# Performance work log

Measured on AMD Instinct MI355X. Metric: run time of the kernel, lower is better.

## Reference

```python
import jax, jax.numpy as jnp
import numpy as np

NUM_HEADS = 16
NUM_KV_HEADS = 4
HEAD_DIM = 256
ROPE_THETA = 10000.0


def _rope(x, position_ids):
    # x: [B, H, S, D], position_ids: [B, S]
    d = x.shape[-1]
    inv_freq = 1.0 / (ROPE_THETA ** (jnp.arange(0, d, 2, dtype=jnp.float32) / d))  # [D/2]
    freqs = position_ids.astype(jnp.float32)[:, :, None] * inv_freq[None, None, :]  # [B, S, D/2]
    emb = jnp.concatenate([freqs, freqs], axis=-1)  # [B, S, D]
    cos = jnp.cos(emb)[:, None, :, :]
    sin = jnp.sin(emb)[:, None, :, :]
    x1, x2 = jnp.split(x, 2, axis=-1)
    rot = jnp.concatenate([-x2, x1], axis=-1)
    return x * cos + rot * sin


def setup_inputs() -> dict:
    key = jax.random.key(0)
    k1, k2, k3, k4, k5 = jax.random.split(key, 5)
    B, S, H = 2, 2048, 2048
    hidden_states = jax.random.normal(k1, (B, S, H), dtype=jnp.float32)
    position_ids = jnp.broadcast_to(jnp.arange(S, dtype=jnp.int32)[None, :], (B, S))
    scale = 1.0 / np.sqrt(H)
    wq = jax.random.normal(k2, (H, NUM_HEADS * HEAD_DIM), dtype=jnp.float32) * scale
    wk = jax.random.normal(k3, (H, NUM_KV_HEADS * HEAD_DIM), dtype=jnp.float32) * scale
    wv = jax.random.normal(k4, (H, NUM_KV_HEADS * HEAD_DIM), dtype=jnp.float32) * scale
    wo = jax.random.normal(k5, (NUM_HEADS * HEAD_DIM, H), dtype=jnp.float32) * (1.0 / np.sqrt(NUM_HEADS * HEAD_DIM))
    return {"hidden_states": hidden_states, "position_ids": position_ids,
            "wq": wq, "wk": wk, "wv": wv, "wo": wo}


def reference(hidden_states, position_ids, wq, wk, wv, wo):
    B, S, H = hidden_states.shape
    groups = NUM_HEADS // NUM_KV_HEADS
    # QKV projections -> [B, heads, S, D]
    q = (hidden_states @ wq).reshape(B, S, NUM_HEADS, HEAD_DIM).transpose(0, 2, 1, 3)
    k = (hidden_states @ wk).reshape(B, S, NUM_KV_HEADS, HEAD_DIM).transpose(0, 2, 1, 3)
    v = (hidden_states @ wv).reshape(B, S, NUM_KV_HEADS, HEAD_DIM).transpose(0, 2, 1, 3)
    q = _rope(q, position_ids)
    k = _rope(k, position_ids)
    # GQA without materializing repeated K/V: group query heads per kv head
    qg = q.reshape(B, NUM_KV_HEADS, groups, S, HEAD_DIM)
    scale = 1.0 / jnp.sqrt(jnp.asarray(HEAD_DIM, dtype=q.dtype))
    scores = jnp.einsum('bkgqd,bkvd->bkgqv', qg, k) * scale  # [B, KV, G, S, S]
    causal = jnp.tril(jnp.ones((S, S), dtype=bool))
    scores = jnp.where(causal[None, None, None, :, :], scores, jnp.finfo(scores.dtype).min)
    probs = jax.nn.softmax(scores, axis=-1)
    out = jnp.einsum('bkgqv,bkvd->bkgqd', probs, v)  # [B, KV, G, S, D]
    out = out.reshape(B, NUM_HEADS, S, HEAD_DIM).transpose(0, 2, 1, 3).reshape(B, S, NUM_HEADS * HEAD_DIM)
    return out @ wo
```

## Files before the change

kernel.cpp:

```cpp
#include <hip/hip_runtime.h>

typedef unsigned short u16;
typedef __bf16 bf16_t;
typedef bf16_t bf16x8 __attribute__((ext_vector_type(8)));
typedef float f32x4 __attribute__((ext_vector_type(4)));
typedef float f32x16 __attribute__((ext_vector_type(16)));

#define LOG2E 1.4426950408889634f
#define QKVS 6144

__device__ __forceinline__ u16 f2bf(float f) {
  union { float f; unsigned u; } c; c.f = f;
  unsigned r = c.u + 0x7fffu + ((c.u >> 16) & 1u);
  return (u16)(r >> 16);
}
__device__ __forceinline__ float bf2f(u16 u) {
  union { unsigned u; float f; } c; c.u = ((unsigned)u) << 16;
  return c.f;
}

__device__ __forceinline__ void gload16(const void* g, void* l) {
  __builtin_amdgcn_global_load_lds(
      (const __attribute__((address_space(1))) unsigned int*)g,
      (__attribute__((address_space(3))) unsigned int*)l, 16, 0, 0);
}

__device__ __forceinline__ unsigned cvtpk(float lo, float hi) {
  unsigned r;
  asm("v_cvt_pk_bf16_f32 %0, %1, %2" : "=v"(r) : "v"(lo), "v"(hi));
  return r;
}
__device__ __forceinline__ void swap32(unsigned& a, unsigned& b) {
  asm("v_permlane32_swap_b32 %0, %1" : "+v"(a), "+v"(b));
}

#define MFMA16(a, b, c) __builtin_amdgcn_mfma_f32_16x16x32_bf16((a), (b), (c), 0, 0, 0)
#define MFMA32(a, b, c) __builtin_amdgcn_mfma_f32_32x32x16_bf16((a), (b), (c), 0, 0, 0)


__global__ __launch_bounds__(256) void k_convert_f32_bf16(const float* __restrict__ in,
                                                          u16* __restrict__ out, int n4) {
  int i = blockIdx.x * 256 + threadIdx.x;
  if (i >= n4) return;
  float4 v = ((const float4*)in)[i];
  ushort4 o;
  o.x = f2bf(v.x); o.y = f2bf(v.y); o.z = f2bf(v.z); o.w = f2bf(v.w);
  ((ushort4*)out)[i] = o;
}

__global__ __launch_bounds__(256) void k_transpose_f32_bf16(const float* __restrict__ in,
                                                            u16* __restrict__ out, int R, int C) {
  __shared__ float tile[32][33];
  int tx = threadIdx.x, ty = threadIdx.y;
  int bx = blockIdx.x * 32, by = blockIdx.y * 32;
#pragma unroll
  for (int i = 0; i < 4; i++)
    tile[ty + i * 8][tx] = in[(size_t)(by + ty + i * 8) * C + bx + tx];
  __syncthreads();
#pragma unroll
  for (int i = 0; i < 4; i++)
    out[(size_t)(bx + ty + i * 8) * R + by + tx] = f2bf(tile[tx][ty + i * 8]);
}

__global__ __launch_bounds__(256) void k_transpose_bf16(const u16* __restrict__ in,
                                                        u16* __restrict__ out, int R, int C) {
  __shared__ u16 tile[32][33];
  int tx = threadIdx.x, ty = threadIdx.y;
  int bx = blockIdx.x * 32, by = blockIdx.y * 32;
#pragma unroll
  for (int i = 0; i < 4; i++)
    tile[ty + i * 8][tx] = in[(size_t)(by + ty + i * 8) * C + bx + tx];
  __syncthreads();
#pragma unroll
  for (int i = 0; i < 4; i++)
    out[(size_t)(bx + ty + i * 8) * R + by + tx] = tile[tx][ty + i * 8];
}

__global__ __launch_bounds__(256) void k_rope(u16* __restrict__ x, const int* __restrict__ pos,
                                              int nh_mask, int nh_shift, int width) {
  int idx = blockIdx.x * 256 + threadIdx.x;
  int i = idx & 127;
  int h = (idx >> 7) & nh_mask;
  int row = idx >> (7 + nh_shift);
  int p = pos[row];
  float f = (float)p * exp2f((float)i * (-13.287712379549449f / 128.f));
  float sn, cs;
  sincosf(f, &sn, &cs);
  size_t base = (size_t)row * width + h * 256 + i;
  float x1 = bf2f(x[base]), x2 = bf2f(x[base + 128]);
  x[base] = f2bf(x1 * cs - x2 * sn);
  x[base + 128] = f2bf(x2 * cs + x1 * sn);
}


template <int OUT_BF16>
__global__ __launch_bounds__(256) void k_gemm_bt(const u16* __restrict__ A,
                                                 const u16* __restrict__ Bt,
                                                 void* __restrict__ C, int M, int N, int K) {
  __shared__ u16 As[128 * 64];
  __shared__ u16 Bs[128 * 64];
  const int tid = threadIdx.x;
  const int lane = tid & 63;
  const int w = tid >> 6;
  const int l15 = lane & 15, l4 = lane >> 4;
  const int wr = w >> 1, wc = w & 1;
  const int bx = blockIdx.x, by = blockIdx.y;

  f32x4 acc[4][4];
#pragma unroll
  for (int a = 0; a < 4; a++)
#pragma unroll
    for (int b2 = 0; b2 < 4; b2++) acc[a][b2] = (f32x4){0.f, 0.f, 0.f, 0.f};

  const u16* Abase = A + (size_t)by * 128 * K;
  const u16* Bbase = Bt + (size_t)bx * 128 * K;

  for (int kk = 0; kk < K; kk += 64) {
    __syncthreads();
#pragma unroll
    for (int j = 0; j < 4; j++) {
      int ci = w * 256 + j * 64 + lane;
      int row = ci >> 3, c = ci & 7;
      gload16(Abase + (size_t)row * K + kk + c * 8, (char*)As + ci * 16);
      gload16(Bbase + (size_t)row * K + kk + c * 8, (char*)Bs + ci * 16);
    }
    __syncthreads();
#pragma unroll
    for (int kc = 0; kc < 2; kc++) {
      int kb = kc * 64 + l4 * 16;
      bf16x8 av[4], bv[4];
#pragma unroll
      for (int mt = 0; mt < 4; mt++)
        av[mt] = *(const bf16x8*)((const char*)As + (wr * 64 + mt * 16 + l15) * 128 + kb);
#pragma unroll
      for (int nt = 0; nt < 4; nt++)
        bv[nt] = *(const bf16x8*)((const char*)Bs + (wc * 64 + nt * 16 + l15) * 128 + kb);
#pragma unroll
      for (int mt = 0; mt < 4; mt++)
#pragma unroll
        for (int nt = 0; nt < 4; nt++) acc[mt][nt] = MFMA16(av[mt], bv[nt], acc[mt][nt]);
    }
  }
#pragma unroll
  for (int mt = 0; mt < 4; mt++) {
#pragma unroll
    for (int nt = 0; nt < 4; nt++) {
      int col = bx * 128 + wc * 64 + nt * 16 + l15;
#pragma unroll
      for (int r = 0; r < 4; r++) {
        int row = by * 128 + wr * 64 + mt * 16 + l4 * 4 + r;
        if (OUT_BF16)
          ((u16*)C)[(size_t)row * N + col] = f2bf(acc[mt][nt][r]);
        else
          ((float*)C)[(size_t)row * N + col] = acc[mt][nt][r];
      }
    }
  }
}


__global__ __launch_bounds__(512, 1) void k_gemm256(const u16* __restrict__ A,
                                                    const u16* __restrict__ Bt,
                                                    u16* __restrict__ C, int N, int K) {
  extern __shared__ char smem[];
  const int tid = threadIdx.x;
  const int lane = tid & 63, w = tid >> 6;
  const int l15 = lane & 15, l4 = lane >> 4;
  const int wr = w >> 2, wc = w & 3;
  const int bx = blockIdx.x, by = blockIdx.y;
  const int NT = K >> 6;

  const u16* Ab = A + (size_t)(by * 256) * K;
  const u16* Bb = Bt + (size_t)(bx * 256) * K;

  int srcoff[2], dstoff[2];
#pragma unroll
  for (int rr = 0; rr < 2; rr++) {
    int ci = rr * 512 + tid;
    int lc = ci ^ (((ci >> 5) & 1) << 1);
    int kc = lc >> 9, row = (lc >> 2) & 127, g2 = lc & 3;
    srcoff[rr] = row * K + kc * 32 + g2 * 8;
    dstoff[rr] = ci * 16;
  }

  auto SH = [&](int Tg, int halfidx) {
    const u16* base = (halfidx < 2) ? (Ab + (size_t)(halfidx * 128) * K)
                                    : (Bb + (size_t)((halfidx - 2) * 128) * K);
    char* dst = smem + (Tg & 1) * 65536 + halfidx * 16384;
    int kk = Tg * 64;
#pragma unroll
    for (int rr = 0; rr < 2; rr++)
      gload16(base + srcoff[rr] + kk, dst + dstoff[rr]);
  };

  auto lda = [&](int c, int kc, int mrow4) -> bf16x8 {
    int L = kc * 8192 + (mrow4 * 16 + l15) * 64 + l4 * 16;
    int P = L ^ (((L >> 9) & 1) << 5);
    return *(const bf16x8*)(smem + c * 65536 + wr * 16384 + P);
  };
  auto ldb = [&](int c, int kc, int j) -> bf16x8 {
    int L = kc * 8192 + ((wc & 1) * 64 + j * 16 + l15) * 64 + l4 * 16;
    int P = L ^ (((L >> 9) & 1) << 5);
    return *(const bf16x8*)(smem + c * 65536 + 32768 + (wc >> 1) * 16384 + P);
  };

  f32x4 acc[8][4];
#pragma unroll
  for (int i = 0; i < 8; i++)
#pragma unroll
    for (int j = 0; j < 4; j++) acc[i][j] = (f32x4){0.f, 0.f, 0.f, 0.f};

  SH(0, 0); SH(0, 1); SH(0, 2); SH(0, 3);
  SH(1, 2); SH(1, 3);
  asm volatile("s_waitcnt vmcnt(4)" ::: "memory");
  __builtin_amdgcn_s_barrier();
  asm volatile("" ::: "memory");

  bf16x8 bv[2][4];
  for (int T = 0; T < NT; ++T) {
    const int c = T & 1;
#pragma unroll
    for (int q = 0; q < 4; q++) {
      const int kc = q & 1, mh = q >> 1;
      bf16x8 av[4];
      if (q < 2) {
#pragma unroll
        for (int j = 0; j < 4; j++) bv[kc][j] = ldb(c, kc, j);
      }
#pragma unroll
      for (int ii = 0; ii < 4; ii++) av[ii] = lda(c, kc, mh * 4 + ii);
      if (q == 0)      { if (T + 1 < NT) SH(T + 1, 0); }
      else if (q == 1) { if (T + 1 < NT) SH(T + 1, 1); }
      else if (q == 2) { if (T + 2 < NT) SH(T + 2, 2); }
      else             { if (T + 2 < NT) SH(T + 2, 3); }
      if (q == 3) {
        if (T < NT - 2)       asm volatile("s_waitcnt vmcnt(4)" ::: "memory");
        else if (T == NT - 2) asm volatile("s_waitcnt vmcnt(0)" ::: "memory");
      }
      asm volatile("" ::: "memory");
      __builtin_amdgcn_s_barrier();
      asm volatile("" ::: "memory");
      asm volatile("s_waitcnt lgkmcnt(0)" ::: "memory");
      __builtin_amdgcn_sched_barrier(0);
      __builtin_amdgcn_s_setprio(1);
#pragma unroll
      for (int ii = 0; ii < 4; ii++)
#pragma unroll
        for (int j = 0; j < 4; j++)
          acc[mh * 4 + ii][j] = MFMA16(av[ii], bv[kc][j], acc[mh * 4 + ii][j]);
      __builtin_amdgcn_s_setprio(0);
      asm volatile("" ::: "memory");
      __builtin_amdgcn_s_barrier();
      asm volatile("" ::: "memory");
    }
  }

#pragma unroll
  for (int i = 0; i < 8; i++) {
#pragma unroll
    for (int j = 0; j < 4; j++) {
      int col = bx * 256 + wc * 64 + j * 16 + l15;
#pragma unroll
      for (int r = 0; r < 4; r++) {
        int row = by * 256 + wr * 128 + i * 16 + l4 * 4 + r;
        C[(size_t)row * N + col] = f2bf(acc[i][j][r]);
      }
    }
  }
}


__shared__ __align__(16) u16 aK0[8192];
__shared__ __align__(16) u16 aK1[8192];
__shared__ __align__(16) u16 aV0[8192];
__shared__ __align__(16) u16 aV1[8192];

__global__ __launch_bounds__(256, 2) void k_attn(const u16* __restrict__ QKV,
                                                 const u16* __restrict__ Vt,
                                                 u16* __restrict__ AO) {
  const int tid = threadIdx.x, lane = tid & 63, w = tid >> 6;
  const int r31 = lane & 31, hi = lane >> 5;

  const int flat = blockIdx.x;
  const int r = flat & 7;
  const int idx = flat >> 3;
  const int b = r >> 2, kv = r & 3;
  const int half = idx >> 5, j = idx & 31;
  const int qb = half ? 15 - (j >> 1) : (j >> 1);
  const int h = kv * 4 + (j & 1) + 2 * half;

  bf16x8 qreg[16];
  {
    const u16* qp = QKV + (size_t)(b * 2048 + qb * 128 + w * 32 + r31) * QKVS + h * 256 + hi * 8;
#pragma unroll
    for (int kc = 0; kc < 16; kc++) qreg[kc] = *(const bf16x8*)(qp + kc * 16);
  }

  f32x16 o[8];
#pragma unroll
  for (int df = 0; df < 8; df++)
#pragma unroll
    for (int jj = 0; jj < 16; jj++) o[df][jj] = 0.f;
  float mrow = -3e38f, lrow = 0.f;

  const int nt = 4 * qb + 4;
  const int tlim = 4 * qb + w;
  const int qloc = qb * 128 + w * 32 + r31;
  const u16* Kbase = QKV + (size_t)(b * 2048) * QKVS + 4096 + kv * 256;
  const u16* Vbase = Vt + (size_t)(kv * 256) * 4096 + b * 2048;

  int kfix[4], vfix[4];
#pragma unroll
  for (int jj = 0; jj < 4; jj++) {
    int ci = jj * 256 + tid;
    int krow = ci >> 5, kc = ci & 31;
    int kcg = (kc & 24) | ((kc ^ krow) & 7);
    kfix[jj] = krow * QKVS + kcg * 8;
    int vrow = ci >> 2, vc = ci & 3;
    int vg = (vc - (vrow >> 1)) & 3;
    vfix[jj] = vrow * 4096 + vg * 8;
  }
  int koff = 0, voff = 0;

  auto STAGE = [&](u16* Kd, u16* Vd) {
#pragma unroll
    for (int jj = 0; jj < 4; jj++)
      gload16(Kbase + kfix[jj] + koff, (char*)Kd + (jj * 256 + tid) * 16);
#pragma unroll
    for (int jj = 0; jj < 4; jj++)
      gload16(Vbase + vfix[jj] + voff, (char*)Vd + (jj * 256 + tid) * 16);
    koff += 32 * QKVS;
    voff += 32;
  };

  auto COMPUTE = [&](int t, const u16* Kc, const u16* Vc) {
    f32x16 s;
#pragma unroll
    for (int jj = 0; jj < 16; jj++) s[jj] = 0.f;
#pragma unroll
    for (int kc = 0; kc < 16; kc++) {
      int ch = kc * 2 + hi;
      int cs = (ch & 24) | ((ch ^ r31) & 7);
      bf16x8 kf = *(const bf16x8*)((const char*)Kc + r31 * 512 + cs * 16);
      s = MFMA32(kf, qreg[kc], s);
    }

    const float C = 0.0625f * LOG2E;
    float z[16];
#pragma unroll
    for (int jj = 0; jj < 16; jj++) z[jj] = s[jj] * C;
    if (t == tlim) {
#pragma unroll
      for (int jj = 0; jj < 16; jj++) {
        int kvg = t * 32 + (jj & 3) + 8 * (jj >> 2) + 4 * hi;
        if (kvg > qloc) z[jj] = -1e30f;
      }
    }

    float m0 = z[0];
#pragma unroll
    for (int jj = 1; jj < 16; jj++) m0 = fmaxf(m0, z[jj]);
    m0 = fmaxf(m0, __shfl_xor(m0, 32));
    if (__any(m0 > mrow + 11.54f)) {
      float mn = fmaxf(mrow, m0);
      float alpha = exp2f(mrow - mn);
      mrow = mn;
      lrow *= alpha;
#pragma unroll
      for (int jj = 0; jj < 16; jj++) {
        float a = __shfl(alpha, (jj & 3) + 8 * (jj >> 2) + 4 * hi);
#pragma unroll
        for (int df = 0; df < 8; df++) o[df][jj] *= a;
      }
    }
    float sum = 0.f;
#pragma unroll
    for (int jj = 0; jj < 16; jj++) {
      z[jj] = exp2f(z[jj] - mrow);
      sum += z[jj];
    }
    sum += __shfl_xor(sum, 32);
    lrow += sum;

    unsigned a0 = cvtpk(z[0], z[1]), a2 = cvtpk(z[4], z[5]);
    swap32(a0, a2);
    unsigned a1 = cvtpk(z[2], z[3]), a3 = cvtpk(z[6], z[7]);
    swap32(a1, a3);
    unsigned b0 = cvtpk(z[8], z[9]), b2 = cvtpk(z[12], z[13]);
    swap32(b0, b2);
    unsigned b1 = cvtpk(z[10], z[11]), b3 = cvtpk(z[14], z[15]);
    swap32(b1, b3);
    union UU { unsigned u[4]; bf16x8 v; };
    UU ua; ua.u[0] = a0; ua.u[1] = a1; ua.u[2] = a2; ua.u[3] = a3;
    UU ub; ub.u[0] = b0; ub.u[1] = b1; ub.u[2] = b2; ub.u[3] = b3;
    bf16x8 pa0 = ua.v, pa1 = ub.v;

#pragma unroll
    for (int df = 0; df < 8; df++) {
      int vr = df * 32 + r31;
      int c0 = (hi + (vr >> 1)) & 3;
      int c1 = (2 + hi + (vr >> 1)) & 3;
      bf16x8 v0 = *(const bf16x8*)((const char*)Vc + vr * 64 + c0 * 16);
      bf16x8 v1 = *(const bf16x8*)((const char*)Vc + vr * 64 + c1 * 16);
      o[df] = MFMA32(pa0, v0, o[df]);
      o[df] = MFMA32(pa1, v1, o[df]);
    }
  };

  STAGE(aK0, aV0);
  __syncthreads();

  for (int t = 0; t < nt; t += 2) {
    STAGE(aK1, aV1);
    if (t <= tlim) COMPUTE(t, aK0, aV0);
    __syncthreads();
    if (t + 2 < nt) STAGE(aK0, aV0);
    if (t + 1 <= tlim) COMPUTE(t + 1, aK1, aV1);
    __syncthreads();
  }

  float rl = 1.f / lrow;
  size_t rowbase = (size_t)(b * 2048 + qb * 128 + w * 32);
#pragma unroll
  for (int jj = 0; jj < 16; jj++) {
    float rr2 = __shfl(rl, (jj & 3) + 8 * (jj >> 2) + 4 * hi);
    int qr = (jj & 3) + 8 * (jj >> 2) + 4 * hi;
#pragma unroll
    for (int df = 0; df < 8; df++)
      AO[(rowbase + qr) * 4096 + h * 256 + df * 32 + r31] = f2bf(o[df][jj] * rr2);
  }
}


#define OFF_AO    0u
#define OFF_XB    0u
#define OFF_WQKVT 16777216u
#define OFF_VT    33554432u
#define OFF_WOT   41943040u
#define OFF_QKV   58720256u

extern "C" void kernel_launch(void* const* d_in, const int* in_sizes, int n_in,
                              void* d_out, int out_size, void* d_ws, size_t ws_size,
                              hipStream_t stream) {
  const float* hs = (const float*)d_in[0];
  const int* pos = (const int*)d_in[1];
  const float* wq = (const float*)d_in[2];
  const float* wk = (const float*)d_in[3];
  const float* wv = (const float*)d_in[4];
  const float* wo = (const float*)d_in[5];
  float* out = (float*)d_out;
  char* ws = (char*)d_ws;

  u16* Xb    = (u16*)(ws + OFF_XB);
  u16* Wqkvt = (u16*)(ws + OFF_WQKVT);
  u16* Vt    = (u16*)(ws + OFF_VT);
  u16* Wot   = (u16*)(ws + OFF_WOT);
  u16* QKV   = (u16*)(ws + OFF_QKV);
  u16* AO    = (u16*)(ws + OFF_AO);

  dim3 tb(32, 8);

  k_convert_f32_bf16<<<8192, 256, 0, stream>>>(hs, Xb, 2097152);
  k_transpose_f32_bf16<<<dim3(128, 64), tb, 0, stream>>>(wq, Wqkvt, 2048, 4096);
  k_transpose_f32_bf16<<<dim3(32, 64), tb, 0, stream>>>(wk, Wqkvt + 4096 * 2048, 2048, 1024);
  k_transpose_f32_bf16<<<dim3(32, 64), tb, 0, stream>>>(wv, Wqkvt + 5120 * 2048, 2048, 1024);
  k_transpose_f32_bf16<<<dim3(64, 128), tb, 0, stream>>>(wo, Wot, 4096, 2048);

  (void)hipFuncSetAttribute((const void*)k_gemm256,
                            hipFuncAttributeMaxDynamicSharedMemorySize, 131072);
  k_gemm256<<<dim3(24, 16), 512, 131072, stream>>>(Xb, Wqkvt, QKV, 6144, 2048);

  k_rope<<<32768, 256, 0, stream>>>(QKV, pos, 15, 4, QKVS);
  k_rope<<<8192, 256, 0, stream>>>(QKV + 4096, pos, 3, 2, QKVS);

  k_transpose_bf16<<<dim3(32, 128), tb, 0, stream>>>(QKV + 5120, Vt, 4096, QKVS);

  k_attn<<<dim3(512), 256, 0, stream>>>(QKV, Vt, AO);

  k_gemm_bt<0><<<dim3(16, 32), 256, 0, stream>>>(AO, Wot, out, 4096, 2048, 4096);
}
```

Baseline: 479.4 us.

## Split heavy causal attention blocks across two wave groups with split-KV merge

The attention kernel now launches 384 blocks of 512 threads instead of 512 blocks of 256. The 256 heavy blocks (query blocks 8-15) split their KV range between two 4-wave groups, each with its own LDS double buffer, and merge the partial softmax states through shared memory at the end. Light blocks (query blocks 0-7) run two heads per block that share one staged KV stream. The aim is to even out the causal load imbalance and the tail effect, at the cost of 128KB of LDS per block, an extra merge step, and occupancy limited to one block per CU.

```diff
diff --git a/kernel.cpp b/kernel.cpp
--- a/kernel.cpp
+++ b/kernel.cpp
@@ -270,24 +270,40 @@
 }
 
 
-__shared__ __align__(16) u16 aK0[8192];
-__shared__ __align__(16) u16 aK1[8192];
-__shared__ __align__(16) u16 aV0[8192];
-__shared__ __align__(16) u16 aV1[8192];
-
-__global__ __launch_bounds__(256, 2) void k_attn(const u16* __restrict__ QKV,
+__global__ __launch_bounds__(512, 1) void k_attn(const u16* __restrict__ QKV,
                                                  const u16* __restrict__ Vt,
                                                  u16* __restrict__ AO) {
-  const int tid = threadIdx.x, lane = tid & 63, w = tid >> 6;
+  __shared__ __align__(16) char sbuf[131072];
+  __shared__ float mlx[256];
+
+  const int tid = threadIdx.x, lane = tid & 63;
+  const int wg = tid >> 6, g = wg >> 2, w = wg & 3;
   const int r31 = lane & 31, hi = lane >> 5;
 
   const int flat = blockIdx.x;
-  const int r = flat & 7;
-  const int idx = flat >> 3;
-  const int b = r >> 2, kv = r & 3;
-  const int half = idx >> 5, j = idx & 31;
-  const int qb = half ? 15 - (j >> 1) : (j >> 1);
-  const int h = kv * 4 + (j & 1) + 2 * half;
+  const bool heavy = flat < 256;
+  int b, kv, qb, h;
+  if (heavy) {
+    int r = flat & 7; b = r >> 2; kv = r & 3;
+    int e = flat >> 3;
+    qb = 15 - (e & 7);
+    h = kv * 4 + (e >> 3);
+  } else {
+    int f2 = flat - 256;
+    int r = f2 & 7; b = r >> 2; kv = r & 3;
+    int e = f2 >> 3;
+    qb = 7 - (e & 7);
+    h = kv * 4 + (e >> 3) * 2 + g;
+  }
+  const int half = heavy ? (2 * qb + 2) : (4 * qb + 4);
+  const int t0 = heavy ? g * half : 0;
+  const bool dostage = heavy || (g == 0);
+
+  char* gb = sbuf + (heavy ? g : 0) * 65536;
+  u16* K0 = (u16*)(gb);
+  u16* K1 = (u16*)(gb + 16384);
+  u16* V0 = (u16*)(gb + 32768);
+  u16* V1 = (u16*)(gb + 49152);
 
   bf16x8 qreg[16];
   {
@@ -303,7 +319,6 @@
     for (int jj = 0; jj < 16; jj++) o[df][jj] = 0.f;
   float mrow = -3e38f, lrow = 0.f;
 
-  const int nt = 4 * qb + 4;
   const int tlim = 4 * qb + w;
   const int qloc = qb * 128 + w * 32 + r31;
   const u16* Kbase = QKV + (size_t)(b * 2048) * QKVS + 4096 + kv * 256;
@@ -312,7 +327,7 @@
   int kfix[4], vfix[4];
 #pragma unroll
   for (int jj = 0; jj < 4; jj++) {
-    int ci = jj * 256 + tid;
+    int ci = jj * 256 + (tid & 255);
     int krow = ci >> 5, kc = ci & 31;
     int kcg = (kc & 24) | ((kc ^ krow) & 7);
     kfix[jj] = krow * QKVS + kcg * 8;
@@ -320,15 +335,15 @@
     int vg = (vc - (vrow >> 1)) & 3;
     vfix[jj] = vrow * 4096 + vg * 8;
   }
-  int koff = 0, voff = 0;
+  int koff = t0 * 32 * QKVS, voff = t0 * 32;
 
   auto STAGE = [&](u16* Kd, u16* Vd) {
 #pragma unroll
     for (int jj = 0; jj < 4; jj++)
-      gload16(Kbase + kfix[jj] + koff, (char*)Kd + (jj * 256 + tid) * 16);
+      gload16(Kbase + kfix[jj] + koff, (char*)Kd + (jj * 256 + (tid & 255)) * 16);
 #pragma unroll
     for (int jj = 0; jj < 4; jj++)
-      gload16(Vbase + vfix[jj] + voff, (char*)Vd + (jj * 256 + tid) * 16);
+      gload16(Vbase + vfix[jj] + voff, (char*)Vd + (jj * 256 + (tid & 255)) * 16);
     koff += 32 * QKVS;
     voff += 32;
   };
@@ -407,27 +422,62 @@
     }
   };
 
-  STAGE(aK0, aV0);
+  if (dostage) STAGE(K0, V0);
   __syncthreads();
 
-  for (int t = 0; t < nt; t += 2) {
-    STAGE(aK1, aV1);
-    if (t <= tlim) COMPUTE(t, aK0, aV0);
+  for (int tt = 0; tt < half; tt += 2) {
+    int t = t0 + tt;
+    if (dostage) STAGE(K1, V1);
+    if (t <= tlim) COMPUTE(t, K0, V0);
     __syncthreads();
-    if (t + 2 < nt) STAGE(aK0, aV0);
-    if (t + 1 <= tlim) COMPUTE(t + 1, aK1, aV1);
+    if (dostage && tt + 2 < half) STAGE(K0, V0);
+    if (t + 1 <= tlim) COMPUTE(t + 1, K1, V1);
     __syncthreads();
   }
 
-  float rl = 1.f / lrow;
-  size_t rowbase = (size_t)(b * 2048 + qb * 128 + w * 32);
-#pragma unroll
-  for (int jj = 0; jj < 16; jj++) {
-    float rr2 = __shfl(rl, (jj & 3) + 8 * (jj >> 2) + 4 * hi);
-    int qr = (jj & 3) + 8 * (jj >> 2) + 4 * hi;
-#pragma unroll
-    for (int df = 0; df < 8; df++)
-      AO[(rowbase + qr) * 4096 + h * 256 + df * 32 + r31] = f2bf(o[df][jj] * rr2);
+  if (!heavy) {
+    float rl = 1.f / lrow;
+    size_t rowbase = (size_t)(b * 2048 + qb * 128 + w * 32);
+#pragma unroll
+    for (int jj = 0; jj < 16; jj++) {
+      float rr2 = __shfl(rl, (jj & 3) + 8 * (jj >> 2) + 4 * hi);
+      int qr = (jj & 3) + 8 * (jj >> 2) + 4 * hi;
+#pragma unroll
+      for (int df = 0; df < 8; df++)
+        AO[(rowbase + qr) * 4096 + h * 256 + df * 32 + r31] = f2bf(o[df][jj] * rr2);
+    }
+  } else {
+    float* X = (float*)sbuf;
+    if (g == 1) {
+      float* xw = X + w * 8192;
+#pragma unroll
+      for (int df = 0; df < 8; df++)
+#pragma unroll
+        for (int jj = 0; jj < 16; jj++) xw[(df * 16 + jj) * 64 + lane] = o[df][jj];
+      if (lane < 32) {
+        mlx[w * 32 + r31] = mrow;
+        mlx[128 + w * 32 + r31] = lrow;
+      }
+    }
+    __syncthreads();
+    if (g == 0) {
+      float m1 = mlx[w * 32 + r31], l1 = mlx[128 + w * 32 + r31];
+      float mm = fmaxf(mrow, m1);
+      float a0 = exp2f(mrow - mm), a1 = exp2f(m1 - mm);
+      float rl = 1.f / (lrow * a0 + l1 * a1);
+      const float* xw = X + w * 8192;
+      size_t rowbase = (size_t)(b * 2048 + qb * 128 + w * 32);
+#pragma unroll
+      for (int jj = 0; jj < 16; jj++) {
+        int qr = (jj & 3) + 8 * (jj >> 2) + 4 * hi;
+        float A0 = __shfl(a0, qr), A1 = __shfl(a1, qr), RL = __shfl(rl, qr);
+#pragma unroll
+        for (int df = 0; df < 8; df++) {
+          float v = o[df][jj] * A0 + xw[(df * 16 + jj) * 64 + lane] * A1;
+          AO[(rowbase + qr) * 4096 + h * 256 + df * 32 + r31] = f2bf(v * RL);
+        }
+      }
+    }
   }
 }
 
@@ -475,7 +525,7 @@
 
   k_transpose_bf16<<<dim3(32, 128), tb, 0, stream>>>(QKV + 5120, Vt, 4096, QKVS);
 
-  k_attn<<<dim3(512), 256, 0, stream>>>(QKV, Vt, AO);
+  k_attn<<<dim3(384), 512, 0, stream>>>(QKV, Vt, AO);
 
   k_gemm_bt<0><<<dim3(16, 32), 256, 0, stream>>>(AO, Wot, out, 4096, 2048, 4096);
 }
```

After: 502.4 us. +4.8%, slower.

## Fuse Q RoPE into attention kernel and batch LDS loads before MFMAs

Applied to the files above, without the earlier changes.

Removes the separate RoPE launch over Q and applies the rotation to the Q registers inside the attention kernel after they are loaded. Each element's frequency and sincos are computed on the fly from the position ids. The QK^T and PV inner loops are also restructured so that eight LDS fragments are loaded before their MFMAs are issued, which should give more latency hiding. The costs are extra transcendental work per attention block and higher register pressure under the launch bound of two blocks per SIMD.

```diff
diff --git a/kernel.cpp b/kernel.cpp
--- a/kernel.cpp
+++ b/kernel.cpp
@@ -277,6 +277,7 @@
 
 __global__ __launch_bounds__(256, 2) void k_attn(const u16* __restrict__ QKV,
                                                  const u16* __restrict__ Vt,
+                                                 const int* __restrict__ pos,
                                                  u16* __restrict__ AO) {
   const int tid = threadIdx.x, lane = tid & 63, w = tid >> 6;
   const int r31 = lane & 31, hi = lane >> 5;
@@ -289,11 +290,33 @@
   const int qb = half ? 15 - (j >> 1) : (j >> 1);
   const int h = kv * 4 + (j & 1) + 2 * half;
 
+  const int qloc = qb * 128 + w * 32 + r31;
+
   bf16x8 qreg[16];
   {
-    const u16* qp = QKV + (size_t)(b * 2048 + qb * 128 + w * 32 + r31) * QKVS + h * 256 + hi * 8;
+    const u16* qp = QKV + (size_t)(b * 2048 + qloc) * QKVS + h * 256 + hi * 8;
 #pragma unroll
     for (int kc = 0; kc < 16; kc++) qreg[kc] = *(const bf16x8*)(qp + kc * 16);
+    float pp = (float)pos[b * 2048 + qloc];
+    union BU { bf16x8 v; u16 a[8]; };
+#pragma unroll
+    for (int kc = 0; kc < 8; kc++) {
+      BU lo, hh;
+      lo.v = qreg[kc];
+      hh.v = qreg[kc + 8];
+#pragma unroll
+      for (int e = 0; e < 8; e++) {
+        int i = kc * 16 + hi * 8 + e;
+        float f = pp * exp2f((float)i * (-13.287712379549449f / 128.f));
+        float sn, cs;
+        sincosf(f, &sn, &cs);
+        float x1 = bf2f(lo.a[e]), x2 = bf2f(hh.a[e]);
+        lo.a[e] = f2bf(x1 * cs - x2 * sn);
+        hh.a[e] = f2bf(x2 * cs + x1 * sn);
+      }
+      qreg[kc] = lo.v;
+      qreg[kc + 8] = hh.v;
+    }
   }
 
   f32x16 o[8];
@@ -305,7 +328,6 @@
 
   const int nt = 4 * qb + 4;
   const int tlim = 4 * qb + w;
-  const int qloc = qb * 128 + w * 32 + r31;
   const u16* Kbase = QKV + (size_t)(b * 2048) * QKVS + 4096 + kv * 256;
   const u16* Vbase = Vt + (size_t)(kv * 256) * 4096 + b * 2048;
 
@@ -338,11 +360,17 @@
 #pragma unroll
     for (int jj = 0; jj < 16; jj++) s[jj] = 0.f;
 #pragma unroll
-    for (int kc = 0; kc < 16; kc++) {
-      int ch = kc * 2 + hi;
-      int cs = (ch & 24) | ((ch ^ r31) & 7);
-      bf16x8 kf = *(const bf16x8*)((const char*)Kc + r31 * 512 + cs * 16);
-      s = MFMA32(kf, qreg[kc], s);
+    for (int hf = 0; hf < 2; hf++) {
+      bf16x8 kb[8];
+#pragma unroll
+      for (int k2 = 0; k2 < 8; k2++) {
+        int kc = hf * 8 + k2;
+        int ch = kc * 2 + hi;
+        int cs = (ch & 24) | ((ch ^ r31) & 7);
+        kb[k2] = *(const bf16x8*)((const char*)Kc + r31 * 512 + cs * 16);
+      }
+#pragma unroll
+      for (int k2 = 0; k2 < 8; k2++) s = MFMA32(kb[k2], qreg[hf * 8 + k2], s);
     }
 
     const float C = 0.0625f * LOG2E;
@@ -396,14 +424,17 @@
     bf16x8 pa0 = ua.v, pa1 = ub.v;
 
 #pragma unroll
-    for (int df = 0; df < 8; df++) {
-      int vr = df * 32 + r31;
-      int c0 = (hi + (vr >> 1)) & 3;
-      int c1 = (2 + hi + (vr >> 1)) & 3;
-      bf16x8 v0 = *(const bf16x8*)((const char*)Vc + vr * 64 + c0 * 16);
-      bf16x8 v1 = *(const bf16x8*)((const char*)Vc + vr * 64 + c1 * 16);
-      o[df] = MFMA32(pa0, v0, o[df]);
-      o[df] = MFMA32(pa1, v1, o[df]);
+    for (int hf = 0; hf < 2; hf++) {
+      bf16x8 vb[8];
+#pragma unroll
+      for (int df = 0; df < 8; df++) {
+        int vr = df * 32 + r31;
+        int cc = (hf * 2 + hi + (vr >> 1)) & 3;
+        vb[df] = *(const bf16x8*)((const char*)Vc + vr * 64 + cc * 16);
+      }
+#pragma unroll
+      for (int df = 0; df < 8; df++)
+        o[df] = MFMA32(hf ? pa1 : pa0, vb[df], o[df]);
     }
   };
 
@@ -470,12 +501,11 @@
                             hipFuncAttributeMaxDynamicSharedMemorySize, 131072);
   k_gemm256<<<dim3(24, 16), 512, 131072, stream>>>(Xb, Wqkvt, QKV, 6144, 2048);
 
-  k_rope<<<32768, 256, 0, stream>>>(QKV, pos, 15, 4, QKVS);
   k_rope<<<8192, 256, 0, stream>>>(QKV + 4096, pos, 3, 2, QKVS);
 
   k_transpose_bf16<<<dim3(32, 128), tb, 0, stream>>>(QKV + 5120, Vt, 4096, QKVS);
 
-  k_attn<<<dim3(512), 256, 0, stream>>>(QKV, Vt, AO);
+  k_attn<<<dim3(512), 256, 0, stream>>>(QKV, Vt, pos, AO);
 
   k_gemm_bt<0><<<dim3(16, 32), 256, 0, stream>>>(AO, Wot, out, 4096, 2048, 4096);
 }
```

New measurement: 470.9 us. About the same (-1.8%).
